# Performance work log

Hardware: AMD Instinct MI355X
Metric: run time of the kernel (lower is better)

The kernel has to match this reference:

```python
import jax, jax.numpy as jnp
import numpy as np
import math

SCALING = math.sqrt(3.0)

def setup_inputs() -> dict:
    key = jax.random.key(0)
    ks = jax.random.split(key, 5)
    B, S, I, H = 32, 1024, 1024, 1024
    std = math.sqrt(3.0 / (3 * H))
    x = jax.random.normal(ks[0], (B, S, I), dtype=jnp.float32)
    w = jax.random.uniform(ks[1], (3 * H, I), dtype=jnp.float32, minval=-std, maxval=std)
    b = jax.random.normal(ks[2], (3 * H,), dtype=jnp.float32) * 0.01
    v_f = jax.random.normal(ks[3], (H,), dtype=jnp.float32) * 0.1
    v_r = jax.random.normal(ks[4], (H,), dtype=jnp.float32) * 0.1
    return {"x": x, "w": w, "b": b, "v_f": v_f, "v_r": v_r}

def reference(x, w, b, v_f, v_r):
    B, S, I = x.shape
    H = v_f.shape[0]
    # big GEMM: [B,S,I] x [I,3H] -> [B,S,3H]
    wx = jnp.einsum('bsi,hi->bsh', x, w) + b
    wf_x = wx[..., :H]
    wc_x = wx[..., H:2 * H]
    wr_x = wx[..., 2 * H:]
    c0 = jnp.zeros((B, H), dtype=x.dtype)

    def step(c, inp):
        wf_t, wc_t = inp  # each [B,H]
        f = jax.nn.sigmoid(wf_t + v_f * c)
        c_new = f * (c - wc_t) + wc_t
        return c_new, (c, c_new)  # (prev_c, c) per step

    # scan over time: transpose to [S,B,H]
    _, (prev_cs, cs) = jax.lax.scan(
        step, c0, (jnp.swapaxes(wf_x, 0, 1), jnp.swapaxes(wc_x, 0, 1)))
    prev_cs = jnp.swapaxes(prev_cs, 0, 1)  # [B,S,H]
    cs = jnp.swapaxes(cs, 0, 1)            # [B,S,H]

    r = jax.nn.sigmoid(wr_x + v_r * prev_cs)
    xs = x * SCALING
    h = r * (cs - xs) + xs
    return h, cs[:, -1]
```

## Files before the change

kernel.cpp:

```cpp
#include <hip/hip_runtime.h>

typedef unsigned short u16;
typedef unsigned int u32;
typedef __attribute__((ext_vector_type(4))) float f32x4;
typedef __attribute__((ext_vector_type(4))) u16 u16x4;
typedef __attribute__((ext_vector_type(8))) u16 u16x8;
typedef __attribute__((ext_vector_type(8))) __bf16 bf16x8;

#define BDIM 32
#define SDIM 1024
#define HDIM 1024
#define MT (BDIM*SDIM)
#define NT (3*HDIM)
#define KT 1024
#define TILE_U (8388608u)

__device__ __forceinline__ float bf2f(u16 u) {
  u32 x = ((u32)u) << 16;
  return __builtin_bit_cast(float, x);
}
__device__ __forceinline__ u16 f2bf(float f) {
  u32 x = __builtin_bit_cast(u32, f);
  x = x + 0x7fffu + ((x >> 16) & 1u);
  return (u16)(x >> 16);
}

typedef __attribute__((address_space(1))) void gvoid;
typedef __attribute__((address_space(3))) void lvoid;
__device__ __forceinline__ void gload16(const u16* g, u16* l) {
  __builtin_amdgcn_global_load_lds((gvoid*)g, (lvoid*)l, 16, 0, 0);
}

__global__ void cast_kernel(const float* __restrict__ in, u16* __restrict__ out, int n4) {
  int idx = blockIdx.x * blockDim.x + threadIdx.x;
  int stride = gridDim.x * blockDim.x;
  const f32x4* in4 = (const f32x4*)in;
  u16x4* out4 = (u16x4*)out;
  for (int i = idx; i < n4; i += stride) {
    f32x4 v = in4[i];
    u16x4 o;
    o[0] = f2bf(v[0]); o[1] = f2bf(v[1]); o[2] = f2bf(v[2]); o[3] = f2bf(v[3]);
    out4[i] = o;
  }
}

__global__ __launch_bounds__(256) void gemm_kernel(
    const u16* __restrict__ A,
    const u16* __restrict__ W,
    const float* __restrict__ bias,
    u16x4* __restrict__ PW,
    u16x4* __restrict__ R)
{
  __shared__ u16 As[128 * 32];
  __shared__ u16 Bs[128 * 32];
  const int tid  = threadIdx.x;
  const int lane = tid & 63;
  const int wave = tid >> 6;

  int bid = blockIdx.x;
  bid = (bid & 7) * 768 + (bid >> 3);
  const int bm = bid / (NT / 128);
  const int bn = bid % (NT / 128);
  const int wm = (wave >> 1) * 64;
  const int wn = (wave & 1) * 64;

  f32x4 acc[4][4] = {};

  const int rsub = lane >> 2;
  const int ksub = (lane & 3) * 8;
  const int c0 = wave * 2;

  const u16* Ab0 = A + (size_t)(bm * 128 + c0 * 16 + rsub) * KT + ksub;
  const u16* Ab1 = A + (size_t)(bm * 128 + (c0 + 1) * 16 + rsub) * KT + ksub;
  const u16* Wb0 = W + (size_t)(bn * 128 + c0 * 16 + rsub) * KT + ksub;
  const u16* Wb1 = W + (size_t)(bn * 128 + (c0 + 1) * 16 + rsub) * KT + ksub;
  u16* lA0 = &As[c0 * 512];
  u16* lA1 = &As[(c0 + 1) * 512];
  u16* lB0 = &Bs[c0 * 512];
  u16* lB1 = &Bs[(c0 + 1) * 512];

  const int fr = lane & 15;
  const int fk = (lane >> 4) * 8;

  for (int kt = 0; kt < KT / 32; ++kt) {
    const int k0 = kt * 32;
    gload16(Ab0 + k0, lA0);
    gload16(Ab1 + k0, lA1);
    gload16(Wb0 + k0, lB0);
    gload16(Wb1 + k0, lB1);
    __syncthreads();

    bf16x8 av[4], bv[4];
#pragma unroll
    for (int mi = 0; mi < 4; ++mi)
      av[mi] = *(const bf16x8*)&As[(wm + mi * 16 + fr) * 32 + fk];
#pragma unroll
    for (int ni = 0; ni < 4; ++ni)
      bv[ni] = *(const bf16x8*)&Bs[(wn + ni * 16 + fr) * 32 + fk];
#pragma unroll
    for (int mi = 0; mi < 4; ++mi)
#pragma unroll
      for (int ni = 0; ni < 4; ++ni)
        acc[mi][ni] = __builtin_amdgcn_mfma_f32_16x16x32_bf16(av[mi], bv[ni], acc[mi][ni], 0, 0, 0);
    __syncthreads();
  }

  const int b_i   = bm >> 3;
  const int trow  = ((bm & 7) << 7) + wm + ((lane >> 4) << 2);
  const int g     = bn >> 3;
  const int hbase = ((bn & 7) << 7) + wn + (lane & 15);

#pragma unroll
  for (int ni = 0; ni < 4; ++ni) {
    const int h  = hbase + ni * 16;
    const int hg = h >> 6;
    const int hl = h & 63;
    const float bb = bias[g * 1024 + h];
#pragma unroll
    for (int mi = 0; mi < 4; ++mi) {
      const int t4 = (trow + mi * 16) >> 2;
      const size_t idx = ((size_t)(b_i * 16 + hg) * 256 + t4) * 64 + hl;
      u16x4 o;
#pragma unroll
      for (int v = 0; v < 4; ++v) o[v] = f2bf(acc[mi][ni][v] + bb);
      if (g < 2) PW[idx * 2 + g] = o;
      else       R[idx] = o;
    }
  }
}

__global__ __launch_bounds__(64) void scan1_kernel(
    const u16x8* __restrict__ PW,
    const float* __restrict__ vf,
    u16x4* __restrict__ Cc,
    float* __restrict__ c_last)
{
  const int lane = threadIdx.x;
  const int bhg  = blockIdx.x;
  const int b    = bhg >> 4;
  const int h    = ((bhg & 15) << 6) + lane;

  const float vfh = vf[h];
  const u16x8* base = PW + (size_t)bhg * 256 * 64 + lane;
  u16x4* cw = Cc + (size_t)bhg * 256 * 64 + lane;

  u16x8 ring[8];
#pragma unroll
  for (int j = 0; j < 8; ++j) ring[j] = base[(size_t)j * 64];

  float c = 0.0f;
#pragma unroll 8
  for (int g = 0; g < 256; ++g) {
    const u16x8 cur = ring[g & 7];
    const int gp = (g + 8 < 256) ? (g + 8) : 255;
    ring[g & 7] = base[(size_t)gp * 64];
    u16x4 oc;
#pragma unroll
    for (int v = 0; v < 4; ++v) {
      const float wf = bf2f(cur[v]);
      const float wc = bf2f(cur[4 + v]);
      const float ef = __expf(-(wf + vfh * c));
      const float f  = 1.0f / (1.0f + ef);
      c = f * (c - wc) + wc;
      oc[v] = f2bf(c);
    }
    cw[(size_t)g * 64] = oc;
  }
  c_last[(size_t)b * HDIM + h] = c;
}

__global__ __launch_bounds__(256) void scan2_kernel(
    const u16x4* __restrict__ R,
    const u16x4* __restrict__ Cc,
    const float* __restrict__ x,
    const float* __restrict__ vr,
    float* __restrict__ h_out)
{
  const int tid = threadIdx.x;
  const int blk = blockIdx.x;
  const int bhg = blk >> 6;
  const int t4  = ((blk & 63) << 2) + (tid >> 6);
  const int hl  = tid & 63;
  const int b   = bhg >> 4;
  const int h   = ((bhg & 15) << 6) + hl;

  const size_t idx = ((size_t)bhg * 256 + t4) * 64 + hl;
  const u16x4 r4 = R[idx];
  const u16x4 c4 = Cc[idx];
  const size_t idxp = (t4 == 0) ? idx : idx - 64;
  const float cprev = (t4 == 0) ? 0.0f : bf2f(Cc[idxp][3]);
  const float vrh = vr[h];
  const float SC = 1.7320508075688772f;

  const float* px = x + ((size_t)b * SDIM + t4 * 4) * HDIM + h;
  float* ph = h_out + ((size_t)b * SDIM + t4 * 4) * HDIM + h;

#pragma unroll
  for (int v = 0; v < 4; ++v) {
    const float cp = (v == 0) ? cprev : bf2f(c4[v - 1]);
    const float er = __expf(-(bf2f(r4[v]) + vrh * cp));
    const float rr = 1.0f / (1.0f + er);
    const float xs = px[(size_t)v * HDIM] * SC;
    ph[(size_t)v * HDIM] = rr * (bf2f(c4[v]) - xs) + xs;
  }
}

extern "C" void kernel_launch(void* const* d_in, const int* in_sizes, int n_in,
                              void* d_out, int out_size, void* d_ws, size_t ws_size,
                              hipStream_t stream) {
  const float* x  = (const float*)d_in[0];
  const float* w  = (const float*)d_in[1];
  const float* b  = (const float*)d_in[2];
  const float* vf = (const float*)d_in[3];
  const float* vr = (const float*)d_in[4];

  float* out    = (float*)d_out;
  float* h_out  = out;
  float* c_last = out + (size_t)33554432;

  char* ws = (char*)d_ws;
  u16*   xb = (u16*)ws;
  u16*   wb = (u16*)(ws + 67108864);
  u16x4* PW = (u16x4*)(ws + 73400320);
  u16x4* R  = (u16x4*)(ws + 73400320 + 134217728);
  u16x4* Cc = (u16x4*)ws;

  cast_kernel<<<4096, 256, 0, stream>>>(x, xb, 8388608);
  cast_kernel<<<1024, 256, 0, stream>>>(w, wb, 786432);
  gemm_kernel<<<(MT / 128) * (NT / 128), 256, 0, stream>>>(xb, wb, b, PW, R);
  scan1_kernel<<<512, 64, 0, stream>>>((const u16x8*)PW, vf, Cc, c_last);
  scan2_kernel<<<32768, 256, 0, stream>>>(R, Cc, x, vr, h_out);
}
```

Before: 612.6 us.

## Stage scan inputs through double-buffered LDS using async global-to-LDS loads

The sequential scan kernel now runs with 256 threads per block. All four waves issue async global_load_lds prefetches of the next 16-step window into a double-buffered shared-memory buffer, while wave 0 runs the recurrence from the current buffer. Before, each lane kept an 8-deep register ring of outstanding global loads. The goal is to hide memory latency on the latency-bound serial scan with deeper, wider prefetch. In exchange it adds a block barrier per window, and three waves sit idle during compute.

```diff
diff --git a/kernel.cpp b/kernel.cpp
--- a/kernel.cpp
+++ b/kernel.cpp
@@ -129,44 +129,64 @@
   }
 }
 
-__global__ __launch_bounds__(64) void scan1_kernel(
-    const u16x8* __restrict__ PW,
+__global__ __launch_bounds__(256) void scan1_kernel(
+    const u16* __restrict__ PW,
     const float* __restrict__ vf,
     u16x4* __restrict__ Cc,
     float* __restrict__ c_last)
 {
-  const int lane = threadIdx.x;
+  __shared__ u16 sbuf[2][16 * 512];
+  const int tid  = threadIdx.x;
+  const int lane = tid & 63;
+  const int wave = tid >> 6;
   const int bhg  = blockIdx.x;
   const int b    = bhg >> 4;
   const int h    = ((bhg & 15) << 6) + lane;
 
+  const u16* gsrc = PW + (size_t)bhg * 131072;
+
+#pragma unroll
+  for (int j = 0; j < 4; ++j) {
+    const int g = wave * 4 + j;
+    gload16(gsrc + (size_t)g * 512 + lane * 8, &sbuf[0][g * 512]);
+  }
+  __syncthreads();
+
   const float vfh = vf[h];
-  const u16x8* base = PW + (size_t)bhg * 256 * 64 + lane;
-  u16x4* cw = Cc + (size_t)bhg * 256 * 64 + lane;
-
-  u16x8 ring[8];
-#pragma unroll
-  for (int j = 0; j < 8; ++j) ring[j] = base[(size_t)j * 64];
-
+  u16x4* cw = Cc + (size_t)bhg * 16384 + lane;
   float c = 0.0f;
-#pragma unroll 8
-  for (int g = 0; g < 256; ++g) {
-    const u16x8 cur = ring[g & 7];
-    const int gp = (g + 8 < 256) ? (g + 8) : 255;
-    ring[g & 7] = base[(size_t)gp * 64];
-    u16x4 oc;
-#pragma unroll
-    for (int v = 0; v < 4; ++v) {
-      const float wf = bf2f(cur[v]);
-      const float wc = bf2f(cur[4 + v]);
-      const float ef = __expf(-(wf + vfh * c));
-      const float f  = 1.0f / (1.0f + ef);
-      c = f * (c - wc) + wc;
-      oc[v] = f2bf(c);
+
+  for (int wnd = 0; wnd < 16; ++wnd) {
+    if (wnd + 1 < 16) {
+      const int nbuf = (wnd + 1) & 1;
+#pragma unroll
+      for (int j = 0; j < 4; ++j) {
+        const int gl = wave * 4 + j;
+        const int g  = (wnd + 1) * 16 + gl;
+        gload16(gsrc + (size_t)g * 512 + lane * 8, &sbuf[nbuf][gl * 512]);
+      }
     }
-    cw[(size_t)g * 64] = oc;
-  }
-  c_last[(size_t)b * HDIM + h] = c;
+    if (wave == 0) {
+      const int cbuf = wnd & 1;
+#pragma unroll
+      for (int gi = 0; gi < 16; ++gi) {
+        const u16x8 cur = *(const u16x8*)&sbuf[cbuf][gi * 512 + lane * 8];
+        u16x4 oc;
+#pragma unroll
+        for (int v = 0; v < 4; ++v) {
+          const float wf = bf2f(cur[v]);
+          const float wc = bf2f(cur[4 + v]);
+          const float ef = __expf(-(wf + vfh * c));
+          const float f  = 1.0f / (1.0f + ef);
+          c = f * (c - wc) + wc;
+          oc[v] = f2bf(c);
+        }
+        cw[(size_t)(wnd * 16 + gi) * 64] = oc;
+      }
+    }
+    __syncthreads();
+  }
+  if (wave == 0) c_last[(size_t)b * HDIM + h] = c;
 }
 
 __global__ __launch_bounds__(256) void scan2_kernel(
@@ -228,6 +248,6 @@
   cast_kernel<<<4096, 256, 0, stream>>>(x, xb, 8388608);
   cast_kernel<<<1024, 256, 0, stream>>>(w, wb, 786432);
   gemm_kernel<<<(MT / 128) * (NT / 128), 256, 0, stream>>>(xb, wb, b, PW, R);
-  scan1_kernel<<<512, 64, 0, stream>>>((const u16x8*)PW, vf, Cc, c_last);
+  scan1_kernel<<<512, 256, 0, stream>>>((const u16*)PW, vf, Cc, c_last);
   scan2_kernel<<<32768, 256, 0, stream>>>(R, Cc, x, vr, h_out);
 }
```

Measured after the change: 611.9 us. No clear change (-0.1%).
